# Optimization experiments

Hardware: AMD Instinct MI355X
Metric: run time of the kernel (lower is better)

Reference implementation:

```python
import jax, jax.numpy as jnp
import numpy as np

B, S, A, E, H, V, P = 128, 256, 8, 300, 300, 50000, 3


def _gru(x, wih, whh, bih, bhh):
    """torch.nn.GRU (single layer, batch_first) with gate order r,z,n."""
    h0 = jnp.zeros((x.shape[0], whh.shape[1]), x.dtype)

    def step(h, xt):
        gi = xt @ wih.T + bih            # [B,3H]
        gh = h @ whh.T + bhh
        ir, iz, in_ = jnp.split(gi, 3, axis=-1)
        hr, hz, hn = jnp.split(gh, 3, axis=-1)
        r = jax.nn.sigmoid(ir + hr)
        z = jax.nn.sigmoid(iz + hz)
        n = jnp.tanh(in_ + r * hn)
        hnew = (1.0 - z) * n + z * h
        return hnew, hnew

    _, ys = jax.lax.scan(step, h0, jnp.swapaxes(x, 0, 1))  # scan over time
    return jnp.swapaxes(ys, 0, 1)                          # [B,S,H]


def setup_inputs() -> dict:
    key = jax.random.key(0)
    ks = jax.random.split(key, 16)
    rn = lambda k, shape, s=0.05: jax.random.normal(k, shape, jnp.float32) * s
    z = lambda *shape: jnp.zeros(shape, jnp.float32)
    return {
        "embed_table": rn(ks[0], (V, E), 1.0),
        "w1": rn(ks[1], (E, 3 * E)), "b1": z(E),
        "w2": rn(ks[2], (1, E)),
        "wm": rn(ks[3], (E, E)), "bm": z(E),
        "wd": rn(ks[4], (P, E)), "bd": z(P),
        "wih_l": rn(ks[5], (3 * H, E)), "whh_l": rn(ks[6], (3 * H, H)),
        "bih_l": z(3 * H), "bhh_l": z(3 * H),
        "wih_r": rn(ks[7], (3 * H, E)), "whh_r": rn(ks[8], (3 * H, H)),
        "bih_r": z(3 * H), "bhh_r": z(3 * H),
        "wml": rn(ks[9], (1, H)), "bml": z(1),
        "wmr": rn(ks[10], (1, H)), "bmr": z(1),
        # all token ids >= 1 so lengths are exactly the padded length (packing == identity)
        "text_raw_indices": jax.random.randint(ks[11], (B, S), 1, V),
        "aspect_indices": jax.random.randint(ks[12], (B, A), 1, V),
        "x_l": jax.random.randint(ks[13], (B, S), 1, V),
        "x_r": jax.random.randint(ks[14], (B, S), 1, V),
    }


def _forward(embed_table, w1, b1, w2, wm, bm, wd, bd,
             wih_l, whh_l, bih_l, bhh_l, wih_r, whh_r, bih_r, bhh_r,
             wml, bml, wmr, bmr, text, aspect, xl, xr):
    memory_len = jnp.sum(text != 0, -1)    # [B]
    aspect_len = jnp.sum(aspect != 0, -1)
    left_len = jnp.sum(xl != 0, -1)

    v_a = jnp.sum(embed_table[aspect], 1) / aspect_len[:, None].astype(jnp.float32)  # [B,E]
    memory = embed_table[text]             # [B,S,E]

    # ---- context attention (attention #1), fully vectorized ----
    ctx_l = _gru(embed_table[xl], wih_l, whh_l, bih_l, bhh_l)  # [B,S,H]
    ctx_r = _gru(embed_table[xr], wih_r, whh_r, bih_r, bhh_r)
    attn_l = jax.nn.sigmoid(jnp.einsum('bsh,h->bs', ctx_l, wml[0]) + bml[0]) + 0.5  # [B,S]
    attn_r = jax.nn.sigmoid(jnp.einsum('bsh,h->bs', ctx_r, wmr[0]) + bmr[0]) + 0.5

    idx = jnp.arange(S)[None, :]                      # [1,S]
    a_start = (left_len - aspect_len)[:, None]        # [B,1]
    a_end = left_len[:, None]
    # attn_r reversed over the first aspect_end positions: attn_rr[i,t] = attn_r[i, a_end-1-t]
    attn_rr = jnp.take_along_axis(attn_r, jnp.clip(a_end - 1 - idx, 0, S - 1), axis=1)
    # attn_l shifted by aspect_start: attn_ls[i,t] = attn_l[i, t - a_start]
    attn_ls = jnp.take_along_axis(attn_l, jnp.clip(idx - a_start, 0, S - 1), axis=1)
    w = jnp.where(idx < a_start, attn_rr,
                  jnp.where(idx < a_end, (attn_rr + attn_ls) * 0.5, attn_ls))
    w = jnp.where(idx < memory_len[:, None], w, 1.0)  # untouched past memory_len
    memory = memory * w[..., None]

    v_s = jnp.sum(memory, 1) / memory_len[:, None].astype(jnp.float32)  # [B,E]

    # ---- content attention (attention #2) ----
    feat = jnp.concatenate([memory,
                            jnp.broadcast_to(v_a[:, None, :], memory.shape),
                            jnp.broadcast_to(v_s[:, None, :], memory.shape)], -1)  # [B,S,3E]
    c = jnp.tanh(feat @ w1.T + b1) @ w2.T             # [B,S,1]
    alpha = jax.nn.softmax(c[..., 0], axis=1)         # [B,S]
    v_ts = jnp.einsum('bse,bs->be', memory, alpha)    # [B,E]

    v_ns = v_ts + v_s                                 # dropout is identity at eval
    v_ms = jnp.tanh(v_ns @ wm.T + bm)
    return jax.nn.softmax(v_ms @ wd.T + bd, axis=-1)  # [B,P]


def reference(embed_table, w1, b1, w2, wm, bm, wd, bd,
              wih_l, whh_l, bih_l, bhh_l, wih_r, whh_r, bih_r, bhh_r,
              wml, bml, wmr, bmr, text_raw_indices, aspect_indices, x_l, x_r):
    return _forward(embed_table, w1, b1, w2, wm, bm, wd, bd,
                    wih_l, whh_l, bih_l, bhh_l, wih_r, whh_r, bih_r, bhh_r,
                    wml, bml, wmr, bmr, text_raw_indices, aspect_indices, x_l, x_r)
```

## Files before the change

kernel.cpp:

```cpp
#include <hip/hip_runtime.h>
#include <hip/hip_bf16.h>
#include <math.h>

#define Bd 128
#define Sd 256
#define Ad 8
#define Ed 300
#define Hd 300
#define EP 320
#define Pd 3
#define UC 5
#define BG 8

typedef __attribute__((ext_vector_type(8))) short bfrag;
typedef __attribute__((ext_vector_type(4))) float f32x4;
typedef __attribute__((ext_vector_type(4))) int i32x4;

#define OFF_LENS   0u
#define OFF_FLAGS  4096u
#define OFF_VA     8192u
#define OFF_VS     172032u
#define OFF_U      335872u
#define OFF_ATTN   499712u
#define OFF_ALPHA  761856u
#define OFF_C      892928u
#define OFF_HF     1024000u
#define OFF_PART   1351680u
#define OFF_WF     11837440u
#define OFF_W1B    14295040u
#define OFF_XF     14499840u
#define OFF_MEMW   14499840u
#define WS_NEEDED  56442880u

__device__ __forceinline__ unsigned short f2bf(float f) {
    __hip_bfloat16 h = __float2bfloat16(f);
    return *reinterpret_cast<unsigned short*>(&h);
}
__device__ __forceinline__ float bf2f(unsigned short u) {
    __hip_bfloat16 h = *reinterpret_cast<__hip_bfloat16*>(&u);
    return __bfloat162float(h);
}
__device__ __forceinline__ float sigm(float x) {
    return __builtin_amdgcn_rcpf(1.f + __expf(-x));
}
__device__ __forceinline__ float fast_tanh(float x) {
    x = fminf(fmaxf(x, -15.f), 15.f);
    float e = __expf(2.f * x);
    return (e - 1.f) * __builtin_amdgcn_rcpf(e + 1.f);
}

__device__ __forceinline__ bfrag l2_load16b(const void* p) {
    bfrag v;
    asm volatile("global_load_dwordx4 %0, %1, off sc0"
                 : "=v"(v) : "v"(p) : "memory");
    return v;
}
__device__ __forceinline__ void l2_store16(void* p, i32x4 v) {
    asm volatile("global_store_dwordx4 %0, %1, off sc0"
                 :: "v"(p), "v"(v) : "memory");
}

__global__ void k_lengths(const int* __restrict__ text, const int* __restrict__ aspect,
                          const int* __restrict__ xl, int* __restrict__ lens) {
    int b = blockIdx.x;
    __shared__ int red[3];
    if (threadIdx.x < 3) red[threadIdx.x] = 0;
    __syncthreads();
    int t = threadIdx.x;
    if (t < Sd) {
        if (text[b*Sd + t] != 0) atomicAdd(&red[0], 1);
        if (xl[b*Sd + t]  != 0) atomicAdd(&red[2], 1);
    }
    if (t < Ad) { if (aspect[b*Ad + t] != 0) atomicAdd(&red[1], 1); }
    __syncthreads();
    if (t < 3) lens[b*4 + t] = red[t];
}

__global__ void k_va(const float* __restrict__ embed, const int* __restrict__ aspect,
                     const int* __restrict__ lens, float* __restrict__ va) {
    int b = blockIdx.x;
    __shared__ int aidx[Ad];
    if (threadIdx.x < Ad) aidx[threadIdx.x] = aspect[b*Ad + threadIdx.x];
    __syncthreads();
    float inv = 1.0f / (float)lens[b*4+1];
    for (int e = threadIdx.x; e < EP; e += blockDim.x) {
        float s = 0.f;
        if (e < Ed) {
            for (int a = 0; a < Ad; ++a) s += embed[(size_t)aidx[a]*Ed + e];
        }
        va[b*EP + e] = s * inv;
    }
}

__global__ void k_xf(const float* __restrict__ embed, const int* __restrict__ xl,
                     const int* __restrict__ xr, unsigned short* __restrict__ XF) {
    int side = blockIdx.x >> 8;
    int t = blockIdx.x & 255;
    const int* xs = side ? xr : xl;
    __shared__ int rows_s[Bd];
    if (threadIdx.x < Bd) rows_s[threadIdx.x] = xs[threadIdx.x*Sd + t];
    __syncthreads();
    unsigned short* dst = XF + ((size_t)(side*Sd + t))*40960;
    for (int idx = threadIdx.x; idx < 40960; idx += 256) {
        int bt = idx / 5120;
        int r1 = idx - bt*5120;
        int kt = r1 / 512;
        int r2 = r1 - kt*512;
        int lane = r2 >> 3, j = r2 & 7;
        int b = bt*16 + (lane & 15);
        int kk = kt*32 + (lane >> 4)*8 + j;
        float v = (kk < Ed) ? embed[(size_t)rows_s[b]*Ed + kk] : 0.f;
        dst[idx] = f2bf(v);
    }
}

__global__ void k_wfrag(const float* __restrict__ wih_l, const float* __restrict__ whh_l,
                        const float* __restrict__ wih_r, const float* __restrict__ whh_r,
                        unsigned short* __restrict__ WF) {
    int bid = blockIdx.x;
    int side = bid / 120;
    int r = bid - side*120;
    int mat = r / 60; r -= mat*60;
    int g = r / 20;
    int ut = r - g*20;
    const float* W = mat ? (side ? whh_r : whh_l) : (side ? wih_r : wih_l);
    unsigned short* dst = WF + (size_t)bid*5120;
    for (int idx = threadIdx.x; idx < 5120; idx += 256) {
        int kt = idx / 512;
        int r2 = idx - kt*512;
        int lane = r2 >> 3, j = r2 & 7;
        int unit = ut*16 + (lane & 15);
        int kk = kt*32 + (lane >> 4)*8 + j;
        float v = (unit < Hd && kk < Ed) ? W[(size_t)(g*Hd + unit)*Ed + kk] : 0.f;
        dst[idx] = f2bf(v);
    }
}

__global__ void k_w1conv(const float* __restrict__ w1, unsigned short* __restrict__ w1b) {
    int idx = blockIdx.x*256 + threadIdx.x;
    if (idx >= EP*EP) return;
    int e = idx / EP, k = idx - e*EP;
    float v = (e < Ed && k < Ed) ? w1[(size_t)e*900 + k] : 0.f;
    w1b[idx] = f2bf(v);
}

__global__ __launch_bounds__(256, 1) void k_gru(
        const unsigned short* __restrict__ WF,
        const unsigned short* __restrict__ XF,
        const float* __restrict__ bih_l, const float* __restrict__ bhh_l,
        const float* __restrict__ bih_r, const float* __restrict__ bhh_r,
        const float* __restrict__ wml, const float* __restrict__ wmr,
        unsigned short* __restrict__ HF,
        float* __restrict__ part, int* __restrict__ flags) {
    int bg = blockIdx.x & 7;
    int r8 = blockIdx.x >> 3;
    int side = r8 & 1;
    int uc = r8 >> 1;
    int tid = threadIdx.x;
    int w = tid >> 6, lane = tid & 63, ul = lane & 15, lq = lane >> 4;
    int utg = uc*4 + w;
    int u = utg*16 + ul;

    const float* bih = side ? bih_r : bih_l;
    const float* bhh = side ? bhh_r : bhh_l;
    const float* wmv = side ? wmr : wml;

    float bR=0.f, bZ=0.f, bNI=0.f, bNH=0.f, wml_r=0.f;
    if (u < Hd) {
        bR = bih[u] + bhh[u];
        bZ = bih[Hd+u] + bhh[Hd+u];
        bNI = bih[2*Hd+u];
        bNH = bhh[2*Hd+u];
        wml_r = wmv[u];
    }

    bfrag wI[3][10], wH[3][10];
    #pragma unroll
    for (int g = 0; g < 3; ++g) {
        const unsigned short* pI = WF + ((size_t)((side*2+0)*3+g)*20 + utg)*5120 + lane*8;
        const unsigned short* pH = WF + ((size_t)((side*2+1)*3+g)*20 + utg)*5120 + lane*8;
        #pragma unroll
        for (int kt = 0; kt < 10; ++kt) {
            wI[g][kt] = *(const bfrag*)(pI + kt*512);
            wH[g][kt] = *(const bfrag*)(pH + kt*512);
        }
    }

    __shared__ __align__(16) unsigned short hn_s[1024];
    int* flg = flags + (side*8 + bg)*8;
    unsigned short* hfb = HF + (size_t)((side*8 + bg)*2)*5120;

    bfrag xcur[10];
    {
        const unsigned short* xp = XF + ((size_t)(side*Sd + 0)*8 + bg)*5120 + lane*8;
        #pragma unroll
        for (int kt = 0; kt < 10; ++kt)
            xcur[kt] = *(const bfrag*)(xp + kt*512);
    }

    float hreg[4] = {0.f,0.f,0.f,0.f};
    const f32x4 zero4 = {0.f,0.f,0.f,0.f};

    #pragma unroll 1
    for (int t = 0; t < Sd; ++t) {
        f32x4 aR = zero4, aZ = zero4, aNI = zero4, aNH = zero4;

        #pragma unroll
        for (int kt = 0; kt < 10; ++kt) {
            aR  = __builtin_amdgcn_mfma_f32_16x16x32_bf16(xcur[kt], wI[0][kt], aR, 0,0,0);
            aZ  = __builtin_amdgcn_mfma_f32_16x16x32_bf16(xcur[kt], wI[1][kt], aZ, 0,0,0);
            aNI = __builtin_amdgcn_mfma_f32_16x16x32_bf16(xcur[kt], wI[2][kt], aNI, 0,0,0);
        }

        bfrag xnx[10];
        {
            int tn = (t+1 < Sd) ? t+1 : Sd-1;
            const unsigned short* xp = XF + ((size_t)(side*Sd + tn)*8 + bg)*5120 + lane*8;
            #pragma unroll
            for (int kt = 0; kt < 10; ++kt)
                xnx[kt] = *(const bfrag*)(xp + kt*512);
        }

        if (t > 0) {
            if (w == 0) {
                while (true) {
                    int v = t;
                    if (lane < UC)
                        v = __hip_atomic_load(flg + lane, __ATOMIC_RELAXED, __HIP_MEMORY_SCOPE_AGENT);
                    if (__all(v >= t)) break;
                }
            }
            __syncthreads();
        }
        asm volatile("" ::: "memory");

        const unsigned short* hg = hfb + (size_t)(t & 1)*5120 + lane*8;
        bfrag hf[10];
        #pragma unroll
        for (int kt = 0; kt < 10; ++kt)
            hf[kt] = l2_load16b(hg + kt*512);
        asm volatile("s_waitcnt vmcnt(0)" ::: "memory");
        __builtin_amdgcn_sched_barrier(0);

        #pragma unroll
        for (int kt = 0; kt < 10; ++kt) {
            aR  = __builtin_amdgcn_mfma_f32_16x16x32_bf16(hf[kt], wH[0][kt], aR, 0,0,0);
            aZ  = __builtin_amdgcn_mfma_f32_16x16x32_bf16(hf[kt], wH[1][kt], aZ, 0,0,0);
            aNH = __builtin_amdgcn_mfma_f32_16x16x32_bf16(hf[kt], wH[2][kt], aNH, 0,0,0);
        }

        {
            int u_local = w*16 + ul;
            int kt_l = u_local >> 5, ko = u_local & 31;
            #pragma unroll
            for (int i = 0; i < 4; ++i) {
                float rr = sigm(aR[i] + bR);
                float zz = sigm(aZ[i] + bZ);
                float nn = fast_tanh(aNI[i] + bNI + rr*(aNH[i] + bNH));
                float hv = (1.f - zz)*nn + zz*hreg[i];
                hreg[i] = hv;
                int rrow = lq*4 + i;
                hn_s[kt_l*512 + (rrow + ((ko>>3)<<4))*8 + (ko&7)] = f2bf(hv);
            }
        }
        #pragma unroll
        for (int kt = 0; kt < 10; ++kt) xcur[kt] = xnx[kt];
        __syncthreads();

        {
            unsigned short* hd = hfb + (size_t)((t+1) & 1)*5120 + uc*1024;
            if (tid < 128)
                l2_store16(hd + (size_t)tid*8, ((const i32x4*)hn_s)[tid]);
        }
        asm volatile("s_waitcnt vmcnt(0)" ::: "memory");
        __syncthreads();
        if (t < Sd-1 && tid == 0)
            __hip_atomic_store(flg + uc, t+1, __ATOMIC_RELAXED, __HIP_MEMORY_SCOPE_AGENT);

        #pragma unroll
        for (int i = 0; i < 4; ++i) {
            float pv = hreg[i] * wml_r;
            pv += __shfl_xor(pv, 1, 64);
            pv += __shfl_xor(pv, 2, 64);
            pv += __shfl_xor(pv, 4, 64);
            pv += __shfl_xor(pv, 8, 64);
            if (ul == 0)
                part[((size_t)((((side*8+bg)*UC + uc)*4 + w)*16) + lq*4 + i)*Sd + t] = pv;
        }
    }
}

__global__ void k_attn(const float* __restrict__ part, const float* __restrict__ bml,
                       const float* __restrict__ bmr, float* __restrict__ attn) {
    int side = blockIdx.x >> 7;
    int b = blockIdx.x & 127;
    int bg = b >> 4, r = b & 15;
    int t = threadIdx.x;
    float s = 0.f;
    for (int c = 0; c < UC*4; ++c)
        s += part[((size_t)(((side*8+bg)*UC*4 + c)*16) + r)*Sd + t];
    float bias = side ? bmr[0] : bml[0];
    attn[(size_t)(side*Bd + b)*Sd + t] = sigm(s + bias) + 0.5f;
}

__global__ void k_wmem(const float* __restrict__ embed, const int* __restrict__ text,
                       const float* __restrict__ attn, const int* __restrict__ lens,
                       unsigned short* __restrict__ memw, float* __restrict__ vs) {
    int b = blockIdx.x;
    __shared__ float w_sh[Sd];
    __shared__ int text_s[Sd];
    int memlen = lens[b*4+0], asplen = lens[b*4+1], leftlen = lens[b*4+2];
    int a_start = leftlen - asplen, a_end = leftlen;
    const float* attl = attn + (size_t)b*Sd;
    const float* attr = attn + (size_t)(Bd + b)*Sd;
    if (threadIdx.x < Sd) {
        int i = threadIdx.x;
        int irr = a_end - 1 - i; irr = irr < 0 ? 0 : (irr > Sd-1 ? Sd-1 : irr);
        int ils = i - a_start;   ils = ils < 0 ? 0 : (ils > Sd-1 ? Sd-1 : ils);
        float arr_ = attr[irr], als = attl[ils];
        float w = (i < a_start) ? arr_ : ((i < a_end) ? 0.5f*(arr_+als) : als);
        if (i >= memlen) w = 1.0f;
        w_sh[i] = w;
        text_s[i] = text[b*Sd + i];
    }
    __syncthreads();
    int e = threadIdx.x;
    float acc = 0.f;
    float invm = 1.0f/(float)lens[b*4+0];
    for (int s = 0; s < Sd; ++s) {
        float v = (e < Ed) ? embed[(size_t)text_s[s]*Ed + e] : 0.f;
        float mw = v * w_sh[s];
        memw[((size_t)b*Sd + s)*EP + e] = f2bf(mw);
        acc += mw;
    }
    vs[b*EP + e] = acc * invm;
}

__global__ void k_u(const float* __restrict__ w1, const float* __restrict__ b1,
                    const float* __restrict__ va, const float* __restrict__ vs,
                    float* __restrict__ u) {
    int b = blockIdx.x;
    __shared__ float va_s[Ed], vs_s[Ed];
    for (int k = threadIdx.x; k < Ed; k += blockDim.x) {
        va_s[k] = va[b*EP+k];
        vs_s[k] = vs[b*EP+k];
    }
    __syncthreads();
    int e = threadIdx.x;
    if (e >= EP) return;
    float acc = 0.f;
    if (e < Ed) {
        acc = b1[e];
        const float* r = w1 + (size_t)e*900;
        for (int k = 0; k < Ed; ++k) acc += va_s[k]*r[300+k];
        for (int k = 0; k < Ed; ++k) acc += vs_s[k]*r[600+k];
    }
    u[b*EP + e] = acc;
}

__global__ __launch_bounds__(256) void k_c(const unsigned short* __restrict__ memw,
                   const unsigned short* __restrict__ w1b,
                   const float* __restrict__ u, const float* __restrict__ w2,
                   float* __restrict__ cout) {
    int b = blockIdx.x >> 2;
    int s0 = (blockIdx.x & 3) * 64;
    __shared__ __align__(16) unsigned short A_s[64*328];
    __shared__ __align__(16) unsigned short Bp_s[EP*32];
    __shared__ float u_s[EP], w2_s[EP];
    for (int i = threadIdx.x; i < EP; i += 256) {
        u_s[i] = u[b*EP + i];
        w2_s[i] = (i < Ed) ? w2[i] : 0.f;
    }
    const unsigned short* Ag = memw + ((size_t)b*Sd + s0)*EP;
    for (int c8 = threadIdx.x; c8 < 64*40; c8 += 256) {
        int r = c8 / 40, kk = (c8 - r*40)*8;
        *(bfrag*)(A_s + r*328 + kk) = *(const bfrag*)(Ag + (size_t)r*EP + kk);
    }

    int wave = threadIdx.x >> 6, lane = threadIdx.x & 63;
    int ul = lane & 15, lq = lane >> 4;
    const f32x4 zero4 = {0.f,0.f,0.f,0.f};
    f32x4 acc[20];
    #pragma unroll
    for (int n = 0; n < 20; ++n) acc[n] = zero4;

    for (int kp = 0; kp < 10; ++kp) {
        __syncthreads();
        for (int c8 = threadIdx.x; c8 < EP*4; c8 += 256) {
            int e = c8 >> 2, kk = (c8 & 3)*8;
            *(bfrag*)(Bp_s + e*32 + kk) = *(const bfrag*)(w1b + (size_t)e*EP + kp*32 + kk);
        }
        __syncthreads();
        bfrag a = *(const bfrag*)(A_s + (wave*16 + ul)*328 + kp*32 + lq*8);
        #pragma unroll
        for (int n = 0; n < 20; ++n) {
            bfrag bb = *(const bfrag*)(Bp_s + (n*16 + ul)*32 + lq*8);
            acc[n] = __builtin_amdgcn_mfma_f32_16x16x32_bf16(a, bb, acc[n], 0, 0, 0);
        }
    }
    float cs[4] = {0.f,0.f,0.f,0.f};
    #pragma unroll
    for (int n = 0; n < 20; ++n) {
        int e = n*16 + ul;
        #pragma unroll
        for (int i = 0; i < 4; ++i)
            cs[i] += w2_s[e] * fast_tanh(acc[n][i] + u_s[e]);
    }
    #pragma unroll
    for (int i = 0; i < 4; ++i) {
        float v = cs[i];
        v += __shfl_xor(v, 1, 64); v += __shfl_xor(v, 2, 64);
        v += __shfl_xor(v, 4, 64); v += __shfl_xor(v, 8, 64);
        if (ul == 0) cout[(size_t)b*Sd + s0 + wave*16 + lq*4 + i] = v;
    }
}

__global__ void k_alpha(const float* __restrict__ cin, float* __restrict__ alpha) {
    int b = blockIdx.x;
    int t = threadIdx.x;
    __shared__ float buf[Sd];
    float v = cin[(size_t)b*Sd + t];
    buf[t] = v; __syncthreads();
    for (int s2 = 128; s2 > 0; s2 >>= 1) {
        if (t < s2) buf[t] = fmaxf(buf[t], buf[t+s2]);
        __syncthreads();
    }
    float mx = buf[0];
    __syncthreads();
    float ex = __expf(v - mx);
    buf[t] = ex; __syncthreads();
    for (int s2 = 128; s2 > 0; s2 >>= 1) {
        if (t < s2) buf[t] += buf[t+s2];
        __syncthreads();
    }
    alpha[(size_t)b*Sd + t] = ex / buf[0];
}

__global__ void k_final(const unsigned short* __restrict__ memw, const float* __restrict__ alpha,
                        const float* __restrict__ vs, const float* __restrict__ wm,
                        const float* __restrict__ bm, const float* __restrict__ wd,
                        const float* __restrict__ bd, float* __restrict__ out) {
    int b = blockIdx.x;
    __shared__ float al_s[Sd];
    __shared__ float vns_s[Ed];
    __shared__ float vms_s[Ed];
    __shared__ float lg_s[Pd];
    if (threadIdx.x < Sd) al_s[threadIdx.x] = alpha[(size_t)b*Sd + threadIdx.x];
    __syncthreads();
    int e = threadIdx.x;
    if (e < Ed) {
        float acc = 0.f;
        const unsigned short* mp = memw + (size_t)b*Sd*EP + e;
        for (int s = 0; s < Sd; ++s) acc += bf2f(mp[(size_t)s*EP]) * al_s[s];
        vns_s[e] = acc + vs[b*EP + e];
    }
    __syncthreads();
    if (e < Ed) {
        float acc = bm[e];
        const float* r = wm + (size_t)e*Ed;
        for (int k = 0; k < Ed; ++k) acc += vns_s[k]*r[k];
        vms_s[e] = fast_tanh(acc);
    }
    __syncthreads();
    if (e < Pd) {
        float acc = bd[e];
        const float* r = wd + (size_t)e*Ed;
        for (int k = 0; k < Ed; ++k) acc += vms_s[k]*r[k];
        lg_s[e] = acc;
    }
    __syncthreads();
    if (e < Pd) {
        float m = fmaxf(lg_s[0], fmaxf(lg_s[1], lg_s[2]));
        float den = __expf(lg_s[0]-m)+__expf(lg_s[1]-m)+__expf(lg_s[2]-m);
        out[b*Pd + e] = __expf(lg_s[e]-m)/den;
    }
}

extern "C" void kernel_launch(void* const* d_in, const int* in_sizes, int n_in,
                              void* d_out, int out_size, void* d_ws, size_t ws_size,
                              hipStream_t stream) {
    const float* embed = (const float*)d_in[0];
    const float* w1    = (const float*)d_in[1];
    const float* b1    = (const float*)d_in[2];
    const float* w2    = (const float*)d_in[3];
    const float* wm    = (const float*)d_in[4];
    const float* bm    = (const float*)d_in[5];
    const float* wd    = (const float*)d_in[6];
    const float* bd    = (const float*)d_in[7];
    const float* wih_l = (const float*)d_in[8];
    const float* whh_l = (const float*)d_in[9];
    const float* bih_l = (const float*)d_in[10];
    const float* bhh_l = (const float*)d_in[11];
    const float* wih_r = (const float*)d_in[12];
    const float* whh_r = (const float*)d_in[13];
    const float* bih_r = (const float*)d_in[14];
    const float* bhh_r = (const float*)d_in[15];
    const float* wml   = (const float*)d_in[16];
    const float* bml   = (const float*)d_in[17];
    const float* wmr   = (const float*)d_in[18];
    const float* bmr   = (const float*)d_in[19];
    const int* text    = (const int*)d_in[20];
    const int* aspect  = (const int*)d_in[21];
    const int* xl      = (const int*)d_in[22];
    const int* xr      = (const int*)d_in[23];

    if (ws_size < (size_t)WS_NEEDED) return;
    char* ws = (char*)d_ws;
    int* lens            = (int*)(ws + OFF_LENS);
    int* flags           = (int*)(ws + OFF_FLAGS);
    float* va            = (float*)(ws + OFF_VA);
    float* vs            = (float*)(ws + OFF_VS);
    float* u             = (float*)(ws + OFF_U);
    float* attn          = (float*)(ws + OFF_ATTN);
    float* alpha         = (float*)(ws + OFF_ALPHA);
    float* c             = (float*)(ws + OFF_C);
    unsigned short* HF   = (unsigned short*)(ws + OFF_HF);
    float* part          = (float*)(ws + OFF_PART);
    unsigned short* WF   = (unsigned short*)(ws + OFF_WF);
    unsigned short* w1b  = (unsigned short*)(ws + OFF_W1B);
    unsigned short* XF   = (unsigned short*)(ws + OFF_XF);
    unsigned short* memw = (unsigned short*)(ws + OFF_MEMW);

    hipMemsetAsync(ws + OFF_FLAGS, 0, 4096, stream);
    hipMemsetAsync(ws + OFF_HF, 0, 327680, stream);

    k_lengths<<<128, 256, 0, stream>>>(text, aspect, xl, lens);
    k_va     <<<128, 320, 0, stream>>>(embed, aspect, lens, va);
    k_xf     <<<512, 256, 0, stream>>>(embed, xl, xr, XF);
    k_wfrag  <<<240, 256, 0, stream>>>(wih_l, whh_l, wih_r, whh_r, WF);
    k_w1conv <<<400, 256, 0, stream>>>(w1, w1b);
    k_gru    <<<80, 256, 0, stream>>>(WF, XF, bih_l, bhh_l, bih_r, bhh_r,
                                      wml, wmr, HF, part, flags);
    k_attn   <<<256, 256, 0, stream>>>(part, bml, bmr, attn);
    k_wmem   <<<128, 320, 0, stream>>>(embed, text, attn, lens, memw, vs);
    k_u      <<<128, 320, 0, stream>>>(w1, b1, va, vs, u);
    k_c      <<<512, 256, 0, stream>>>(memw, w1b, u, w2, c);
    k_alpha  <<<128, 256, 0, stream>>>(c, alpha);
    k_final  <<<128, 320, 0, stream>>>(memw, alpha, vs, wm, bm, wd, bd, (float*)d_out);
}
```

Before: 899.2 us.

## Poll GRU step flags via L2 atomics and ping-pong input fragments

The cross-block step handshake now polls a per-chunk counter with an atomic fetch_add of zero, which goes to L2. The agent-scope flag is kept as a fallback read every 64 spins. The time loop is unrolled by two so the x fragments alternate between two register buffers instead of being copied each step. The next-step x prefetch now comes after the flag publish. The intent is to cut handshake latency on the serial recurrence. The risks are that the counters must start from zero every launch, and that workgroup-scope atomics used across blocks rely on hardware behaviour.

After: 865.3 us. -3.8%, faster.

```diff
diff --git a/kernel.cpp b/kernel.cpp
--- a/kernel.cpp
+++ b/kernel.cpp
@@ -187,107 +187,110 @@
     }
 
     __shared__ __align__(16) unsigned short hn_s[1024];
-    int* flg = flags + (side*8 + bg)*8;
+    int* flgL2 = flags + (side*8 + bg)*16;
+    int* flgIC = flags + 512 + (side*8 + bg)*16;
     unsigned short* hfb = HF + (size_t)((side*8 + bg)*2)*5120;
-
-    bfrag xcur[10];
-    {
-        const unsigned short* xp = XF + ((size_t)(side*Sd + 0)*8 + bg)*5120 + lane*8;
-        #pragma unroll
-        for (int kt = 0; kt < 10; ++kt)
-            xcur[kt] = *(const bfrag*)(xp + kt*512);
-    }
+    const unsigned short* xbase = XF + ((size_t)side*Sd*8 + bg)*5120 + lane*8;
+
+    bfrag xA[10], xB[10];
+    #pragma unroll
+    for (int kt = 0; kt < 10; ++kt)
+        xA[kt] = *(const bfrag*)(xbase + 0 + kt*512);
 
     float hreg[4] = {0.f,0.f,0.f,0.f};
     const f32x4 zero4 = {0.f,0.f,0.f,0.f};
 
+#define GRU_STEP(T, XIN, XOUT) do {                                            \
+    f32x4 aR = zero4, aZ = zero4, aNI = zero4, aNH = zero4;                    \
+    _Pragma("unroll")                                                          \
+    for (int kt = 0; kt < 10; ++kt) {                                          \
+        aR  = __builtin_amdgcn_mfma_f32_16x16x32_bf16(XIN[kt], wI[0][kt], aR, 0,0,0); \
+        aZ  = __builtin_amdgcn_mfma_f32_16x16x32_bf16(XIN[kt], wI[1][kt], aZ, 0,0,0); \
+        aNI = __builtin_amdgcn_mfma_f32_16x16x32_bf16(XIN[kt], wI[2][kt], aNI, 0,0,0); \
+    }                                                                          \
+    if ((T) > 0) {                                                             \
+        if (w == 0) {                                                          \
+            int iters = 0;                                                     \
+            while (true) {                                                     \
+                int v = (T);                                                   \
+                if (lane < UC)                                                 \
+                    v = __hip_atomic_fetch_add(flgL2 + lane, 0, __ATOMIC_RELAXED, __HIP_MEMORY_SCOPE_WORKGROUP); \
+                if (__all(v >= (T))) break;                                    \
+                if (((++iters) & 63) == 0) {                                   \
+                    int vv = (T);                                              \
+                    if (lane < UC)                                             \
+                        vv = __hip_atomic_load(flgIC + lane, __ATOMIC_RELAXED, __HIP_MEMORY_SCOPE_AGENT); \
+                    if (__all(vv >= (T))) break;                               \
+                }                                                              \
+            }                                                                  \
+        }                                                                      \
+        __syncthreads();                                                       \
+    }                                                                          \
+    asm volatile("" ::: "memory");                                             \
+    const unsigned short* hg = hfb + (size_t)((T) & 1)*5120 + lane*8;          \
+    bfrag hf[10];                                                              \
+    _Pragma("unroll")                                                          \
+    for (int kt = 0; kt < 10; ++kt)                                            \
+        hf[kt] = l2_load16b(hg + kt*512);                                      \
+    asm volatile("s_waitcnt vmcnt(0)" ::: "memory");                           \
+    __builtin_amdgcn_sched_barrier(0);                                         \
+    _Pragma("unroll")                                                          \
+    for (int kt = 0; kt < 10; ++kt) {                                          \
+        aR  = __builtin_amdgcn_mfma_f32_16x16x32_bf16(hf[kt], wH[0][kt], aR, 0,0,0); \
+        aZ  = __builtin_amdgcn_mfma_f32_16x16x32_bf16(hf[kt], wH[1][kt], aZ, 0,0,0); \
+        aNH = __builtin_amdgcn_mfma_f32_16x16x32_bf16(hf[kt], wH[2][kt], aNH, 0,0,0); \
+    }                                                                          \
+    {                                                                          \
+        int u_local = w*16 + ul;                                               \
+        int kt_l = u_local >> 5, ko = u_local & 31;                            \
+        _Pragma("unroll")                                                      \
+        for (int i = 0; i < 4; ++i) {                                          \
+            float rr = sigm(aR[i] + bR);                                       \
+            float zz = sigm(aZ[i] + bZ);                                       \
+            float nn = fast_tanh(aNI[i] + bNI + rr*(aNH[i] + bNH));            \
+            float hv = (1.f - zz)*nn + zz*hreg[i];                             \
+            hreg[i] = hv;                                                      \
+            int rrow = lq*4 + i;                                               \
+            hn_s[kt_l*512 + (rrow + ((ko>>3)<<4))*8 + (ko&7)] = f2bf(hv);      \
+        }                                                                      \
+    }                                                                          \
+    __syncthreads();                                                           \
+    {                                                                          \
+        unsigned short* hd = hfb + (size_t)(((T)+1) & 1)*5120 + uc*1024;       \
+        if (tid < 128)                                                         \
+            l2_store16(hd + (size_t)tid*8, ((const i32x4*)hn_s)[tid]);         \
+    }                                                                          \
+    asm volatile("s_waitcnt vmcnt(0)" ::: "memory");                           \
+    __syncthreads();                                                           \
+    if ((T) < Sd-1 && tid == 0) {                                              \
+        __hip_atomic_fetch_add(flgL2 + uc, 1, __ATOMIC_RELAXED, __HIP_MEMORY_SCOPE_WORKGROUP); \
+        __hip_atomic_store(flgIC + uc, (T)+1, __ATOMIC_RELAXED, __HIP_MEMORY_SCOPE_AGENT); \
+    }                                                                          \
+    {                                                                          \
+        int tn = ((T)+1 < Sd) ? (T)+1 : Sd-1;                                  \
+        const unsigned short* xp = xbase + (size_t)tn*40960;                   \
+        _Pragma("unroll")                                                      \
+        for (int kt = 0; kt < 10; ++kt)                                        \
+            XOUT[kt] = *(const bfrag*)(xp + kt*512);                           \
+    }                                                                          \
+    _Pragma("unroll")                                                          \
+    for (int i = 0; i < 4; ++i) {                                              \
+        float pv = hreg[i] * wml_r;                                            \
+        pv += __shfl_xor(pv, 1, 64);                                           \
+        pv += __shfl_xor(pv, 2, 64);                                           \
+        pv += __shfl_xor(pv, 4, 64);                                           \
+        pv += __shfl_xor(pv, 8, 64);                                           \
+        if (ul == 0)                                                           \
+            part[((size_t)((((side*8+bg)*UC + uc)*4 + w)*16) + lq*4 + i)*Sd + (T)] = pv; \
+    }                                                                          \
+} while (0)
+
     #pragma unroll 1
-    for (int t = 0; t < Sd; ++t) {
-        f32x4 aR = zero4, aZ = zero4, aNI = zero4, aNH = zero4;
-
-        #pragma unroll
-        for (int kt = 0; kt < 10; ++kt) {
-            aR  = __builtin_amdgcn_mfma_f32_16x16x32_bf16(xcur[kt], wI[0][kt], aR, 0,0,0);
-            aZ  = __builtin_amdgcn_mfma_f32_16x16x32_bf16(xcur[kt], wI[1][kt], aZ, 0,0,0);
-            aNI = __builtin_amdgcn_mfma_f32_16x16x32_bf16(xcur[kt], wI[2][kt], aNI, 0,0,0);
-        }
-
-        bfrag xnx[10];
-        {
-            int tn = (t+1 < Sd) ? t+1 : Sd-1;
-            const unsigned short* xp = XF + ((size_t)(side*Sd + tn)*8 + bg)*5120 + lane*8;
-            #pragma unroll
-            for (int kt = 0; kt < 10; ++kt)
-                xnx[kt] = *(const bfrag*)(xp + kt*512);
-        }
-
-        if (t > 0) {
-            if (w == 0) {
-                while (true) {
-                    int v = t;
-                    if (lane < UC)
-                        v = __hip_atomic_load(flg + lane, __ATOMIC_RELAXED, __HIP_MEMORY_SCOPE_AGENT);
-                    if (__all(v >= t)) break;
-                }
-            }
-            __syncthreads();
-        }
-        asm volatile("" ::: "memory");
-
-        const unsigned short* hg = hfb + (size_t)(t & 1)*5120 + lane*8;
-        bfrag hf[10];
-        #pragma unroll
-        for (int kt = 0; kt < 10; ++kt)
-            hf[kt] = l2_load16b(hg + kt*512);
-        asm volatile("s_waitcnt vmcnt(0)" ::: "memory");
-        __builtin_amdgcn_sched_barrier(0);
-
-        #pragma unroll
-        for (int kt = 0; kt < 10; ++kt) {
-            aR  = __builtin_amdgcn_mfma_f32_16x16x32_bf16(hf[kt], wH[0][kt], aR, 0,0,0);
-            aZ  = __builtin_amdgcn_mfma_f32_16x16x32_bf16(hf[kt], wH[1][kt], aZ, 0,0,0);
-            aNH = __builtin_amdgcn_mfma_f32_16x16x32_bf16(hf[kt], wH[2][kt], aNH, 0,0,0);
-        }
-
-        {
-            int u_local = w*16 + ul;
-            int kt_l = u_local >> 5, ko = u_local & 31;
-            #pragma unroll
-            for (int i = 0; i < 4; ++i) {
-                float rr = sigm(aR[i] + bR);
-                float zz = sigm(aZ[i] + bZ);
-                float nn = fast_tanh(aNI[i] + bNI + rr*(aNH[i] + bNH));
-                float hv = (1.f - zz)*nn + zz*hreg[i];
-                hreg[i] = hv;
-                int rrow = lq*4 + i;
-                hn_s[kt_l*512 + (rrow + ((ko>>3)<<4))*8 + (ko&7)] = f2bf(hv);
-            }
-        }
-        #pragma unroll
-        for (int kt = 0; kt < 10; ++kt) xcur[kt] = xnx[kt];
-        __syncthreads();
-
-        {
-            unsigned short* hd = hfb + (size_t)((t+1) & 1)*5120 + uc*1024;
-            if (tid < 128)
-                l2_store16(hd + (size_t)tid*8, ((const i32x4*)hn_s)[tid]);
-        }
-        asm volatile("s_waitcnt vmcnt(0)" ::: "memory");
-        __syncthreads();
-        if (t < Sd-1 && tid == 0)
-            __hip_atomic_store(flg + uc, t+1, __ATOMIC_RELAXED, __HIP_MEMORY_SCOPE_AGENT);
-
-        #pragma unroll
-        for (int i = 0; i < 4; ++i) {
-            float pv = hreg[i] * wml_r;
-            pv += __shfl_xor(pv, 1, 64);
-            pv += __shfl_xor(pv, 2, 64);
-            pv += __shfl_xor(pv, 4, 64);
-            pv += __shfl_xor(pv, 8, 64);
-            if (ul == 0)
-                part[((size_t)((((side*8+bg)*UC + uc)*4 + w)*16) + lq*4 + i)*Sd + t] = pv;
-        }
-    }
+    for (int tt = 0; tt < Sd; tt += 2) {
+        GRU_STEP(tt,   xA, xB);
+        GRU_STEP(tt+1, xB, xA);
+    }
+#undef GRU_STEP
 }
 
 __global__ void k_attn(const float* __restrict__ part, const float* __restrict__ bml,
```
